# Kernel optimization log

Hardware: AMD Instinct MI355X
Metric: run time of the kernel (lower is better)

Reference implementation:

```python
import jax, jax.numpy as jnp
import numpy as np

M_FUZZ = 2.0        # self.m
EPSILON = 1e-8      # self.Epsilon
MAX_ITER = 25       # self.max_iterion


def setup_inputs() -> dict:
    key = jax.random.key(0)
    k1, k2 = jax.random.split(key)
    data = jax.random.normal(k1, (300000, 64), dtype=jnp.float32)
    u0_raw = jax.random.uniform(k2, (300000, 64), dtype=jnp.float32)
    return {"data": data, "u0_raw": u0_raw, "cluster": 64}


def reference(data, u0_raw, cluster):
    # Fuzzy c-means, faithful to GranularComputing.forward:
    #   iterate: C = center(U); U = update(U, C); C_new = center(U);
    #            stop if ||C_new - C||_F < Epsilon; return C (pre-update center).
    m = M_FUZZ
    p = 2.0 / (m - 1.0)  # exponent in membership update (== 2.0)
    N, D = data.shape

    # initialize_matrix_U: random rows normalized to sum to 1
    U0 = u0_raw / jnp.sum(u0_raw, axis=1, keepdims=True)  # [N, c]

    def center(U):
        Um = U ** m                                        # [N, c]
        num = Um.T @ data                                  # [c, D]
        den = jnp.sum(Um, axis=0)[:, None]                 # [c, 1]
        return num / den

    x2 = jnp.sum(data * data, axis=1, keepdims=True)       # [N, 1]

    def sqdist(C):
        # squared Euclidean distances [N, c] via expansion (no N x c x D tensor)
        c2 = jnp.sum(C * C, axis=1)                        # [c]
        return jnp.maximum(x2 + c2 - 2.0 * (data @ C.T), 0.0)

    def step(carry, _):
        U, C_ret, done = carry
        C = center(U)                                      # [c, D]
        # u_ij = 1 / sum_k (d_ij / d_ik)^p  ==  d_ij^{-p} / sum_k d_ik^{-p}
        w = sqdist(C) ** (-p / 2.0)                        # [N, c]
        U_new = w / jnp.sum(w, axis=1, keepdims=True)
        C_new = center(U_new)
        diff = jnp.sqrt(jnp.sum((C_new - C) ** 2))
        # freeze state after convergence (emulates the early break)
        U_out = jnp.where(done, U, U_new)
        C_out = jnp.where(done, C_ret, C)
        return (U_out, C_out, done | (diff < EPSILON)), None

    C0 = jnp.zeros((cluster, D), dtype=data.dtype)
    (_, V, _), _ = jax.lax.scan(
        step, (U0, C0, jnp.array(False)), None, length=MAX_ITER + 1
    )
    return V  # [cluster, D]
```

## Files before the change

### kernel.cpp

```cpp
#include <hip/hip_runtime.h>


#define DM 64
#define CL 64
#define PARTIAL_STRIDE 4160
#define MAX_ITER 25
#define MAX_BLOCKS 768
#define LDP 72

typedef __attribute__((ext_vector_type(8))) short bf16x8;
typedef __attribute__((ext_vector_type(4))) float f32x4;

__device__ __forceinline__ unsigned f2bf1(float f) {
  unsigned u = __builtin_bit_cast(unsigned, f);
  return (u + 0x7FFFu + ((u >> 16) & 1u)) >> 16;
}
__device__ __forceinline__ unsigned pkbf(float a, float b) {
  return f2bf1(a) | (f2bf1(b) << 16);
}
__device__ __forceinline__ unsigned cvtpk_bf16(float a, float b) {
  unsigned r;
  asm("v_cvt_pk_bf16_f32 %0, %1, %2" : "=v"(r) : "v"(a), "v"(b));
  return r;
}

__device__ __forceinline__ float wave_sum(float v) {
#define DPPADD(ctrl, rmask)                                                  \
  v += __builtin_bit_cast(float, __builtin_amdgcn_update_dpp(                \
           0, __builtin_bit_cast(int, v), ctrl, rmask, 0xf, false));
  DPPADD(0x111, 0xf)
  DPPADD(0x112, 0xf)
  DPPADD(0x114, 0xf)
  DPPADD(0x118, 0xf)
  DPPADD(0x142, 0xa)
  DPPADD(0x143, 0xc)
#undef DPPADD
  return __builtin_bit_cast(
      float, __builtin_amdgcn_readlane(__builtin_bit_cast(int, v), 63));
}

__device__ __forceinline__ float group16_sum(float v) {
#define DPPADD(ctrl)                                                         \
  v += __builtin_bit_cast(float, __builtin_amdgcn_update_dpp(                \
           0, __builtin_bit_cast(int, v), ctrl, 0xf, 0xf, false));
  DPPADD(0xB1)
  DPPADD(0x4E)
  DPPADD(0x141)
  DPPADD(0x140)
#undef DPPADD
  return v;
}

__global__ __launch_bounds__(256)
void fcm_prep(const float* __restrict__ data, float* __restrict__ x2,
              unsigned short* __restrict__ xbf,
              float* __restrict__ diffac, int* __restrict__ done,
              int* __restrict__ ticket, int N) {
  size_t i = (size_t)blockIdx.x * blockDim.x + threadIdx.x;
  if (i == 0) { *diffac = 0.0f; *done = 0; *ticket = 0; }
  size_t nvec = (size_t)N * (DM / 4);
  if (i >= nvec) return;
  float4 v = ((const float4*)data)[i];
  float s = fmaf(v.x, v.x, fmaf(v.y, v.y, fmaf(v.z, v.z, v.w * v.w)));
  float rs = group16_sum(s);
  if ((threadIdx.x & 15) == 0) x2[i >> 4] = rs;
  uint2 pk = {cvtpk_bf16(v.x, v.y), cvtpk_bf16(v.z, v.w)};
  ((uint2*)xbf)[i] = pk;
}

template <bool INIT>
__global__ __launch_bounds__(256, 3)
void fcm_pass(const unsigned short* __restrict__ xbf, const float* __restrict__ x2,
              const float* __restrict__ CU,
              float* __restrict__ partial, const int* __restrict__ done,
              int N, int ntiles) {
  if (!INIT && *done) return;
  __shared__ __align__(16) unsigned short Xb[64 * LDP];
  __shared__ __align__(16) unsigned short XTb[64 * LDP];
  __shared__ __align__(16) unsigned short umT[64 * LDP];
  __shared__ __align__(16) float rpart[4 * 64];
  __shared__ __align__(16) float rrs[64];
  __shared__ __align__(16) float x2s[64];

  const int tid  = threadIdx.x;
  const int w    = __builtin_amdgcn_readfirstlane(tid >> 6);
  const int col  = tid & 15;
  const int quad = (tid >> 4) & 3;

  bf16x8 cf0, cf1;
  float c2j = 0.0f;
  if (!INIT) {
    const float* crow = CU + (size_t)(16 * w + col) * DM;
    float4 ca = *(const float4*)(crow + quad * 8);
    float4 cb = *(const float4*)(crow + quad * 8 + 4);
    float4 cc = *(const float4*)(crow + 32 + quad * 8);
    float4 cd = *(const float4*)(crow + 32 + quad * 8 + 4);
    float cp = ca.x*ca.x + ca.y*ca.y + ca.z*ca.z + ca.w*ca.w
             + cb.x*cb.x + cb.y*cb.y + cb.z*cb.z + cb.w*cb.w
             + cc.x*cc.x + cc.y*cc.y + cc.z*cc.z + cc.w*cc.w
             + cd.x*cd.x + cd.y*cd.y + cd.z*cd.z + cd.w*cd.w;
    cp += __shfl_xor(cp, 16, 64);
    cp += __shfl_xor(cp, 32, 64);
    c2j = cp;
    union { bf16x8 v; unsigned u[4]; } P0, P1;
    P0.u[0] = pkbf(ca.x, ca.y); P0.u[1] = pkbf(ca.z, ca.w);
    P0.u[2] = pkbf(cb.x, cb.y); P0.u[3] = pkbf(cb.z, cb.w);
    P1.u[0] = pkbf(cc.x, cc.y); P1.u[1] = pkbf(cc.z, cc.w);
    P1.u[2] = pkbf(cd.x, cd.y); P1.u[3] = pkbf(cd.z, cd.w);
    cf0 = P0.v; cf1 = P1.v;
  }

  union { bf16x8 v; unsigned u[4]; } ON;
  ON.u[0] = ON.u[1] = ON.u[2] = ON.u[3] = 0x3F803F80u;
  const bf16x8 onesf = ON.v;

  f32x4 D2[4];
#pragma unroll
  for (int dt = 0; dt < 4; dt++) D2[dt] = f32x4{0.f, 0.f, 0.f, 0.f};
  f32x4 Dden = f32x4{0.f, 0.f, 0.f, 0.f};

  const int sp  = tid & 63;
  const int sd0 = (tid >> 6) * 8;
  const unsigned short* gsrc = xbf + (size_t)sp * DM + sd0;
  unsigned short* xw = &Xb[sp * LDP + sd0];
  unsigned short* xt = &XTb[sd0 * LDP + sp];

  for (int t = blockIdx.x; t < ntiles; t += gridDim.x) {
    const int base = t * 64;
    const int np = min(64, N - base);
    __syncthreads();

    {
      bf16x8 v0 = {0, 0, 0, 0, 0, 0, 0, 0};
      bf16x8 v1 = {0, 0, 0, 0, 0, 0, 0, 0};
      if (sp < np) {
        const unsigned short* g = gsrc + (size_t)base * DM;
        v0 = *(const bf16x8*)(g);
        v1 = *(const bf16x8*)(g + 32);
      }
      *(bf16x8*)(void*)xw = v0;
      *(bf16x8*)(void*)(xw + 32) = v1;
#pragma unroll
      for (int k = 0; k < 8; k++) xt[k * LDP] = (unsigned short)v0[k];
#pragma unroll
      for (int k = 0; k < 8; k++) xt[(k + 32) * LDP] = (unsigned short)v1[k];
    }
    if (tid < 64) x2s[tid] = (base + tid < N) ? x2[base + tid] : 0.0f;
    __syncthreads();

    f32x4 Wv[4];
    if (INIT) {
#pragma unroll
      for (int pt = 0; pt < 4; pt++) {
        f32x4 wv = {0.f, 0.f, 0.f, 0.f};
#pragma unroll
        for (int r = 0; r < 4; r++) {
          int pl = pt * 16 + quad * 4 + r;
          if (pl < np) wv[r] = CU[(size_t)(base + pl) * CL + 16 * w + col];
        }
        Wv[pt] = wv;
      }
    } else {
#pragma unroll
      for (int pt = 0; pt < 4; pt++) {
        bf16x8 a0 = *(const bf16x8*)(const void*)&Xb[(pt * 16 + col) * LDP + quad * 8];
        bf16x8 a1 = *(const bf16x8*)(const void*)&Xb[(pt * 16 + col) * LDP + 32 + quad * 8];
        f32x4 s = f32x4{0.f, 0.f, 0.f, 0.f};
        s = __builtin_amdgcn_mfma_f32_16x16x32_bf16(a0, cf0, s, 0, 0, 0);
        s = __builtin_amdgcn_mfma_f32_16x16x32_bf16(a1, cf1, s, 0, 0, 0);
        f32x4 x2v = *(const f32x4*)(const void*)&x2s[pt * 16 + quad * 4];
#pragma unroll
        for (int r = 0; r < 4; r++) {
          float dist = fmaxf(fmaf(-2.0f, s[r], x2v[r] + c2j), 0.0f);
          Wv[pt][r] = __builtin_amdgcn_rcpf(dist);
        }
      }
    }

#pragma unroll
    for (int pt = 0; pt < 4; pt++) {
      float r0 = group16_sum(Wv[pt][0]);
      float r1 = group16_sum(Wv[pt][1]);
      float r2 = group16_sum(Wv[pt][2]);
      float r3 = group16_sum(Wv[pt][3]);
      if (col == 0) {
        float4 v4 = {r0, r1, r2, r3};
        *(float4*)(void*)&rpart[w * 64 + pt * 16 + quad * 4] = v4;
      }
    }
    __syncthreads();
    if (tid < 64) {
      float rt = rpart[tid] + rpart[64 + tid] + rpart[128 + tid] + rpart[192 + tid];
      rrs[tid] = (base + tid < N) ? __builtin_amdgcn_rcpf(rt) : 0.0f;
    }
    __syncthreads();

#pragma unroll
    for (int pt = 0; pt < 4; pt++) {
      f32x4 rrv = *(const f32x4*)(const void*)&rrs[pt * 16 + quad * 4];
      f32x4 u = Wv[pt] * rrv;
      f32x4 m = u * u;
      uint2 pk = {cvtpk_bf16(m[0], m[1]), cvtpk_bf16(m[2], m[3])};
      *(uint2*)(void*)&umT[(16 * w + col) * LDP + pt * 16 + quad * 4] = pk;
    }

#pragma unroll
    for (int pb = 0; pb < 2; pb++) {
      bf16x8 au = *(const bf16x8*)(const void*)&umT[(16 * w + col) * LDP + pb * 32 + quad * 8];
      Dden = __builtin_amdgcn_mfma_f32_16x16x32_bf16(au, onesf, Dden, 0, 0, 0);
#pragma unroll
      for (int dt = 0; dt < 4; dt++) {
        bf16x8 bx = *(const bf16x8*)(const void*)&XTb[(dt * 16 + col) * LDP + pb * 32 + quad * 8];
        D2[dt] = __builtin_amdgcn_mfma_f32_16x16x32_bf16(au, bx, D2[dt], 0, 0, 0);
      }
    }
  }

  float* pbuf = partial + (size_t)blockIdx.x * PARTIAL_STRIDE;
  if (col == 0) {
    float4 dv = {Dden[0], Dden[1], Dden[2], Dden[3]};
    *(float4*)(void*)&pbuf[CL * DM + 16 * w + quad * 4] = dv;
  }
#pragma unroll
  for (int dt = 0; dt < 4; dt++)
#pragma unroll
    for (int r = 0; r < 4; r++)
      pbuf[(size_t)(16 * w + quad * 4 + r) * DM + dt * 16 + col] = D2[dt][r];
}

__global__ __launch_bounds__(1024, 1)
void fcm_reduce(const float* __restrict__ partial, float* __restrict__ Cnew,
                const float* __restrict__ Cold, float* __restrict__ out,
                float* __restrict__ diffac, int* __restrict__ done,
                int* __restrict__ ticket, int compute_diff, int nb) {
  if (compute_diff && *done) return;
  __shared__ float sm[16 * 64];
  __shared__ float sden[1024];
  __shared__ int lastflag;
  __shared__ float sdiff;
  int j = blockIdx.x;
  int tid = threadIdx.x;
  int d = tid & 63;
  int slice = tid >> 6;
  float s = 0.0f;
  for (int b = slice; b < nb; b += 16)
    s += partial[(size_t)b * PARTIAL_STRIDE + j * DM + d];
  sm[slice * 64 + d] = s;
  float dv = 0.0f;
  for (int b = tid; b < nb; b += 1024)
    dv += partial[(size_t)b * PARTIAL_STRIDE + CL * DM + j];
  sden[tid] = dv;
  __syncthreads();
#pragma unroll
  for (int st = 8; st; st >>= 1) {
    if (slice < st) sm[slice * 64 + d] += sm[(slice + st) * 64 + d];
    __syncthreads();
  }
#pragma unroll
  for (int st = 512; st >= 64; st >>= 1) {
    if (tid < st) sden[tid] += sden[tid + st];
    __syncthreads();
  }
  if (tid < 64) {
    float denj = wave_sum(sden[tid]);
    float c = sm[tid] / denj;
    Cnew[j * DM + tid] = c;
    if (compute_diff) {
      float df = c - Cold[j * DM + tid];
      float tot = wave_sum(df * df);
      if (tid == 0) atomicAdd(diffac, tot);
    }
  }
  if (!compute_diff) return;
  __syncthreads();
  if (tid == 0) {
    __threadfence();
    int t = atomicAdd(ticket, 1);
    lastflag = (t == (int)gridDim.x - 1);
  }
  __syncthreads();
  if (!lastflag) return;
  if (tid == 0) sdiff = atomicAdd(diffac, 0.0f);
  __syncthreads();
  if (sdiff < 1e-16f) {
    for (int i = tid; i < CL * DM; i += 1024) out[i] = Cold[i];
    if (tid == 0) *done = 1;
  }
  if (tid == 0) { *diffac = 0.0f; *ticket = 0; }
}

__global__ void fcm_final(const float* __restrict__ Clast, float* __restrict__ out,
                          const int* __restrict__ done) {
  if (*done) return;
  int i = blockIdx.x * blockDim.x + threadIdx.x;
  if (i < CL * DM) out[i] = Clast[i];
}

extern "C" void kernel_launch(void* const* d_in, const int* in_sizes, int n_in,
                              void* d_out, int out_size, void* d_ws, size_t ws_size,
                              hipStream_t stream) {
  const float* data = (const float*)d_in[0];
  const float* u0   = (const float*)d_in[1];
  float* out = (float*)d_out;
  int N = in_sizes[0] / DM;
  int ntiles = (N + 63) / 64;

  float* ws = (float*)d_ws;
  size_t Noff = ((size_t)N + 15) & ~(size_t)15;
  float* x2 = ws;
  unsigned short* xbf = (unsigned short*)(ws + Noff);
  float* C0 = ws + Noff + (size_t)N * 32;
  float* C1 = C0 + CL * DM;
  float* diffac = C1 + CL * DM;
  int* done = (int*)(diffac + 1);
  int* ticket = (int*)(diffac + 2);
  float* partial = diffac + 16;

  size_t used = Noff + (size_t)N * 32 + 2 * CL * DM + 16;
  size_t avail = (ws_size / 4 > used) ? (ws_size / 4 - used) / PARTIAL_STRIDE : 0;
  int nb = (int)(avail < MAX_BLOCKS ? avail : MAX_BLOCKS);
  if (nb < 1) nb = 1;

  size_t nvec = (size_t)N * (DM / 4);
  hipLaunchKernelGGL(fcm_prep, dim3((unsigned)((nvec + 255) / 256)), dim3(256), 0,
                     stream, data, x2, xbf, diffac, done, ticket, N);
  hipLaunchKernelGGL((fcm_pass<true>), dim3(nb), dim3(256), 0, stream,
                     xbf, x2, u0, partial, done, N, ntiles);
  hipLaunchKernelGGL(fcm_reduce, dim3(64), dim3(1024), 0, stream,
                     partial, C0, C1, out, diffac, done, ticket, 0, nb);

  float* bufs[2] = {C0, C1};
  for (int k = 0; k < MAX_ITER; k++) {
    float* Cc = bufs[k & 1];
    float* Cn = bufs[(k + 1) & 1];
    hipLaunchKernelGGL((fcm_pass<false>), dim3(nb), dim3(256), 0, stream,
                       xbf, x2, Cc, partial, done, N, ntiles);
    hipLaunchKernelGGL(fcm_reduce, dim3(64), dim3(1024), 0, stream,
                       partial, Cn, Cc, out, diffac, done, ticket, 1, nb);
  }
  hipLaunchKernelGGL(fcm_final, dim3(16), dim3(256), 0, stream,
                     bufs[1], out, done);
}
```

Measured before the change: 389.6 us.

## Split distance tile by points per wave to make row normalization wave-local

Each wave now owns 16 points and computes distances against all 64 clusters, holding all four center fragments in registers, instead of owning 16 clusters across all points. Because every point's row now lives in one wave, the membership normalization is done with in-wave shuffles, which removes the shared-memory partial-sum buffers and one of the two block barriers per tile. In exchange each thread keeps four times as many center fragments in registers, which raises register pressure and may lower occupancy.

```diff
diff --git a/kernel.cpp b/kernel.cpp
--- a/kernel.cpp
+++ b/kernel.cpp
@@ -78,8 +78,6 @@
   __shared__ __align__(16) unsigned short Xb[64 * LDP];
   __shared__ __align__(16) unsigned short XTb[64 * LDP];
   __shared__ __align__(16) unsigned short umT[64 * LDP];
-  __shared__ __align__(16) float rpart[4 * 64];
-  __shared__ __align__(16) float rrs[64];
   __shared__ __align__(16) float x2s[64];
 
   const int tid  = threadIdx.x;
@@ -87,27 +85,30 @@
   const int col  = tid & 15;
   const int quad = (tid >> 4) & 3;
 
-  bf16x8 cf0, cf1;
-  float c2j = 0.0f;
+  bf16x8 cf0[4], cf1[4];
+  float c2v[4];
   if (!INIT) {
-    const float* crow = CU + (size_t)(16 * w + col) * DM;
-    float4 ca = *(const float4*)(crow + quad * 8);
-    float4 cb = *(const float4*)(crow + quad * 8 + 4);
-    float4 cc = *(const float4*)(crow + 32 + quad * 8);
-    float4 cd = *(const float4*)(crow + 32 + quad * 8 + 4);
-    float cp = ca.x*ca.x + ca.y*ca.y + ca.z*ca.z + ca.w*ca.w
-             + cb.x*cb.x + cb.y*cb.y + cb.z*cb.z + cb.w*cb.w
-             + cc.x*cc.x + cc.y*cc.y + cc.z*cc.z + cc.w*cc.w
-             + cd.x*cd.x + cd.y*cd.y + cd.z*cd.z + cd.w*cd.w;
-    cp += __shfl_xor(cp, 16, 64);
-    cp += __shfl_xor(cp, 32, 64);
-    c2j = cp;
-    union { bf16x8 v; unsigned u[4]; } P0, P1;
-    P0.u[0] = pkbf(ca.x, ca.y); P0.u[1] = pkbf(ca.z, ca.w);
-    P0.u[2] = pkbf(cb.x, cb.y); P0.u[3] = pkbf(cb.z, cb.w);
-    P1.u[0] = pkbf(cc.x, cc.y); P1.u[1] = pkbf(cc.z, cc.w);
-    P1.u[2] = pkbf(cd.x, cd.y); P1.u[3] = pkbf(cd.z, cd.w);
-    cf0 = P0.v; cf1 = P1.v;
+#pragma unroll
+    for (int jt = 0; jt < 4; jt++) {
+      const float* crow = CU + (size_t)(16 * jt + col) * DM;
+      float4 ca = *(const float4*)(crow + quad * 8);
+      float4 cb = *(const float4*)(crow + quad * 8 + 4);
+      float4 cc = *(const float4*)(crow + 32 + quad * 8);
+      float4 cd = *(const float4*)(crow + 32 + quad * 8 + 4);
+      float cp = ca.x*ca.x + ca.y*ca.y + ca.z*ca.z + ca.w*ca.w
+               + cb.x*cb.x + cb.y*cb.y + cb.z*cb.z + cb.w*cb.w
+               + cc.x*cc.x + cc.y*cc.y + cc.z*cc.z + cc.w*cc.w
+               + cd.x*cd.x + cd.y*cd.y + cd.z*cd.z + cd.w*cd.w;
+      cp += __shfl_xor(cp, 16, 64);
+      cp += __shfl_xor(cp, 32, 64);
+      c2v[jt] = cp;
+      union { bf16x8 v; unsigned u[4]; } P0, P1;
+      P0.u[0] = pkbf(ca.x, ca.y); P0.u[1] = pkbf(ca.z, ca.w);
+      P0.u[2] = pkbf(cb.x, cb.y); P0.u[3] = pkbf(cb.z, cb.w);
+      P1.u[0] = pkbf(cc.x, cc.y); P1.u[1] = pkbf(cc.z, cc.w);
+      P1.u[2] = pkbf(cd.x, cd.y); P1.u[3] = pkbf(cd.z, cd.w);
+      cf0[jt] = P0.v; cf1[jt] = P1.v;
+    }
   }
 
   union { bf16x8 v; unsigned u[4]; } ON;
@@ -148,61 +149,51 @@
     if (tid < 64) x2s[tid] = (base + tid < N) ? x2[base + tid] : 0.0f;
     __syncthreads();
 
-    f32x4 Wv[4];
+    float Wv[4][4];
     if (INIT) {
 #pragma unroll
-      for (int pt = 0; pt < 4; pt++) {
-        f32x4 wv = {0.f, 0.f, 0.f, 0.f};
+      for (int jt = 0; jt < 4; jt++)
 #pragma unroll
         for (int r = 0; r < 4; r++) {
-          int pl = pt * 16 + quad * 4 + r;
-          if (pl < np) wv[r] = CU[(size_t)(base + pl) * CL + 16 * w + col];
+          int pl = 16 * w + quad * 4 + r;
+          Wv[jt][r] = (pl < np)
+              ? CU[(size_t)(base + pl) * CL + 16 * jt + col] : 0.0f;
         }
-        Wv[pt] = wv;
-      }
     } else {
-#pragma unroll
-      for (int pt = 0; pt < 4; pt++) {
-        bf16x8 a0 = *(const bf16x8*)(const void*)&Xb[(pt * 16 + col) * LDP + quad * 8];
-        bf16x8 a1 = *(const bf16x8*)(const void*)&Xb[(pt * 16 + col) * LDP + 32 + quad * 8];
+      bf16x8 a0 = *(const bf16x8*)(const void*)&Xb[(16 * w + col) * LDP + quad * 8];
+      bf16x8 a1 = *(const bf16x8*)(const void*)&Xb[(16 * w + col) * LDP + 32 + quad * 8];
+      f32x4 x2p = *(const f32x4*)(const void*)&x2s[16 * w + quad * 4];
+#pragma unroll
+      for (int jt = 0; jt < 4; jt++) {
         f32x4 s = f32x4{0.f, 0.f, 0.f, 0.f};
-        s = __builtin_amdgcn_mfma_f32_16x16x32_bf16(a0, cf0, s, 0, 0, 0);
-        s = __builtin_amdgcn_mfma_f32_16x16x32_bf16(a1, cf1, s, 0, 0, 0);
-        f32x4 x2v = *(const f32x4*)(const void*)&x2s[pt * 16 + quad * 4];
+        s = __builtin_amdgcn_mfma_f32_16x16x32_bf16(a0, cf0[jt], s, 0, 0, 0);
+        s = __builtin_amdgcn_mfma_f32_16x16x32_bf16(a1, cf1[jt], s, 0, 0, 0);
 #pragma unroll
         for (int r = 0; r < 4; r++) {
-          float dist = fmaxf(fmaf(-2.0f, s[r], x2v[r] + c2j), 0.0f);
-          Wv[pt][r] = __builtin_amdgcn_rcpf(dist);
+          float dist = fmaxf(fmaf(-2.0f, s[r], x2p[r] + c2v[jt]), 0.0f);
+          Wv[jt][r] = __builtin_amdgcn_rcpf(dist);
         }
       }
     }
 
-#pragma unroll
-    for (int pt = 0; pt < 4; pt++) {
-      float r0 = group16_sum(Wv[pt][0]);
-      float r1 = group16_sum(Wv[pt][1]);
-      float r2 = group16_sum(Wv[pt][2]);
-      float r3 = group16_sum(Wv[pt][3]);
-      if (col == 0) {
-        float4 v4 = {r0, r1, r2, r3};
-        *(float4*)(void*)&rpart[w * 64 + pt * 16 + quad * 4] = v4;
-      }
-    }
-    __syncthreads();
-    if (tid < 64) {
-      float rt = rpart[tid] + rpart[64 + tid] + rpart[128 + tid] + rpart[192 + tid];
-      rrs[tid] = (base + tid < N) ? __builtin_amdgcn_rcpf(rt) : 0.0f;
-    }
-    __syncthreads();
-
-#pragma unroll
-    for (int pt = 0; pt < 4; pt++) {
-      f32x4 rrv = *(const f32x4*)(const void*)&rrs[pt * 16 + quad * 4];
-      f32x4 u = Wv[pt] * rrv;
-      f32x4 m = u * u;
-      uint2 pk = {cvtpk_bf16(m[0], m[1]), cvtpk_bf16(m[2], m[3])};
-      *(uint2*)(void*)&umT[(16 * w + col) * LDP + pt * 16 + quad * 4] = pk;
-    }
+    float rr[4];
+#pragma unroll
+    for (int r = 0; r < 4; r++) {
+      float rs = Wv[0][r] + Wv[1][r] + Wv[2][r] + Wv[3][r];
+      rs = group16_sum(rs);
+      int pl = 16 * w + quad * 4 + r;
+      rr[r] = (pl < np) ? __builtin_amdgcn_rcpf(rs) : 0.0f;
+    }
+
+#pragma unroll
+    for (int jt = 0; jt < 4; jt++) {
+      float u0v = Wv[jt][0] * rr[0], u1v = Wv[jt][1] * rr[1];
+      float u2v = Wv[jt][2] * rr[2], u3v = Wv[jt][3] * rr[3];
+      uint2 pk = {cvtpk_bf16(u0v * u0v, u1v * u1v),
+                  cvtpk_bf16(u2v * u2v, u3v * u3v)};
+      *(uint2*)(void*)&umT[(16 * jt + col) * LDP + 16 * w + quad * 4] = pk;
+    }
+    __syncthreads();
 
 #pragma unroll
     for (int pb = 0; pb < 2; pb++) {
```

Result: no change. 387.6 us (-0.5%).
